# Kernel optimization log

Measured on AMD Instinct MI355X. Metric: run time of the kernel, lower is better.

The kernel has to match this reference:

```python
import math
import jax, jax.numpy as jnp
import numpy as np

N_HEADS = 32
N_KV_HEADS = 8
HEAD_DIM = 64
DIM = 2048
SEQ = 4096
EST_Q = 64          # idx = min(64, seqlen)
VERTICAL_SIZE = 300 # min(prompt_len, max(300, 30))
SLASH_SIZE = 800    # min(prompt_len, max(800, 50))


def apply_rope(t, cos, sin):
    # t: [B,S,H,hd]; pairs are consecutive (reshape(...,-1,2) in torch view_as_complex)
    B, S, H, hd = t.shape
    tr = t.reshape(B, S, H, hd // 2, 2)
    xr, xi = tr[..., 0], tr[..., 1]
    c = cos[None, :, None, :]
    s = sin[None, :, None, :]
    orr = xr * c - xi * s
    oii = xr * s + xi * c
    return jnp.stack([orr, oii], axis=-1).reshape(B, S, H, hd)


def sum_all_diagonal(mat):
    # faithful jax version of torch as_strided trick: sum over anti-shifted diagonals
    # mat: [b,h,n,m] -> [b,h,n+m-1]; sum_diags[j] = sum_i mat[i, i + j - n], j in [1, n+m-1]
    b, h, n, m = mat.shape
    padded = jnp.pad(mat, ((0, 0), (0, 0), (0, 0), (n, n)))
    gidx = jnp.arange(n)[:, None] + jnp.arange(n + m)[None, :]  # [n, n+m]
    diags = jnp.take_along_axis(padded, jnp.broadcast_to(gidx, (b, h, n, n + m)), axis=-1)
    return diags.sum(axis=2)[:, :, 1:]


def setup_inputs() -> dict:
    key = jax.random.key(0)
    ks = jax.random.split(key, 6)
    x = jax.random.normal(ks[0], (1, SEQ, DIM), dtype=jnp.float32)
    # real RoPE tables (theta = 10000)
    inv_freq = 1.0 / (10000.0 ** (np.arange(0, HEAD_DIM, 2, dtype=np.float32) / HEAD_DIM))
    ang = np.outer(np.arange(SEQ, dtype=np.float32), inv_freq)  # [S, hd/2]
    freqs_cos = jnp.asarray(np.cos(ang), dtype=jnp.float32)
    freqs_sin = jnp.asarray(np.sin(ang), dtype=jnp.float32)
    scale = 0.02
    wq = jax.random.normal(ks[1], (DIM, N_HEADS * HEAD_DIM), dtype=jnp.float32) * scale
    wk = jax.random.normal(ks[2], (DIM, N_KV_HEADS * HEAD_DIM), dtype=jnp.float32) * scale
    wv = jax.random.normal(ks[3], (DIM, N_KV_HEADS * HEAD_DIM), dtype=jnp.float32) * scale
    wo = jax.random.normal(ks[4], (N_HEADS * HEAD_DIM, DIM), dtype=jnp.float32) * scale
    return {"x": x, "freqs_cos": freqs_cos, "freqs_sin": freqs_sin,
            "wq": wq, "wk": wk, "wv": wv, "wo": wo}


def reference(x, freqs_cos, freqs_sin, wq, wk, wv, wo):
    B, S, D = x.shape
    H, Hkv, hd = N_HEADS, N_KV_HEADS, HEAD_DIM
    rep = H // Hkv
    scale = 1.0 / math.sqrt(hd)

    # QKV + RoPE (K gets RoPE, V does not), GQA repeat
    q = apply_rope((x @ wq).reshape(B, S, H, hd), freqs_cos, freqs_sin).transpose(0, 2, 1, 3)
    k = apply_rope((x @ wk).reshape(B, S, Hkv, hd), freqs_cos, freqs_sin)
    v = (x @ wv).reshape(B, S, Hkv, hd)
    k = jnp.repeat(k, rep, axis=2).transpose(0, 2, 1, 3)  # [B,H,S,hd]
    v = jnp.repeat(v, rep, axis=2).transpose(0, 2, 1, 3)

    # --- vertical / slash pattern estimation (first idx queries, as in source) ---
    idx = min(EST_Q, S)
    qe = q[:, :, :idx, :]
    est = jnp.einsum('bhqd,bhkd->bhqk', qe, k) * scale  # [B,H,idx,S]
    ar = jnp.arange(idx)
    blk = ar[:, None] >= ar[None, :]
    tail = jnp.where(blk[None, None], est[..., -idx:], -jnp.inf)
    est = jnp.concatenate([est[..., :S - idx], tail], axis=-1)
    probs = jax.nn.softmax(est, axis=-1)

    Vn = min(S, VERTICAL_SIZE)
    Sl = min(S, SLASH_SIZE)
    vertical = probs.sum(axis=2)                  # [B,H,S]
    _, v_idx = jax.lax.top_k(vertical, Vn)        # [B,H,Vn]
    diag = sum_all_diagonal(probs)[..., :S]       # [..., :-idx+1] -> length S
    _, s_idx = jax.lax.top_k(diag, Sl)
    slash = S - 1 - s_idx                         # [B,H,Sl]

    sparse_keys = jnp.sort(jnp.concatenate([v_idx, slash], axis=-1), axis=-1)  # [B,H,K]

    # --- sparse causal attention over selected keys ---
    k_sp = jnp.take_along_axis(k, sparse_keys[..., None], axis=2)  # [B,H,K,hd]
    v_sp = jnp.take_along_axis(v, sparse_keys[..., None], axis=2)
    att = jnp.einsum('bhqd,bhkd->bhqk', q, k_sp) * scale           # [B,H,S,K]
    causal = sparse_keys[:, :, None, :] <= jnp.arange(S)[None, None, :, None]
    att = jnp.where(causal, att, -1e30)
    p = jax.nn.softmax(att, axis=-1)
    out = jnp.einsum('bhqk,bhkd->bhqd', p, v_sp)
    out = out.transpose(0, 2, 1, 3).reshape(B, S, H * hd)
    return out @ wo
```

## Files before the change

### kernel.cpp

```cpp
#include <hip/hip_runtime.h>
#include <hip/hip_bf16.h>
#include <math.h>
#include <stdint.h>

#define SEQ   4096
#define DIMM  2048
#define NH    32
#define NKV   8
#define HD    64
#define NSP   1100
#define NSPP  1152

typedef __bf16 bf16x8 __attribute__((ext_vector_type(8)));
typedef float  f32x4  __attribute__((ext_vector_type(4)));

#define MODE_V 0
#define MODE_Q 1
#define MODE_O 2

__device__ inline void split8(const float* __restrict__ p, bf16x8& h, bf16x8& l) {
#pragma unroll
    for (int i = 0; i < 8; ++i) {
        float v = p[i];
        __bf16 hv = (__bf16)v;
        h[i] = hv;
        l[i] = (__bf16)(v - (float)hv);
    }
}
__device__ inline f32x4 load4(const void* __restrict__ p, size_t idx, bool f) {
    if (f) return *(const f32x4*)((const float*)p + idx);
    const __bf16* b = (const __bf16*)p + idx;
    f32x4 v;
    v[0] = (float)b[0]; v[1] = (float)b[1]; v[2] = (float)b[2]; v[3] = (float)b[3];
    return v;
}
__device__ __forceinline__ void gl_lds16(const __bf16* __restrict__ g, __bf16* l) {
    __builtin_amdgcn_global_load_lds(
        (const __attribute__((address_space(1))) void*)g,
        (__attribute__((address_space(3))) void*)l, 16, 0, 0);
}
__device__ __forceinline__ void cs_at(const void* fc, const void* fs, bool f,
                                      int t, int j, float& c, float& s) {
    if (f) {
        c = ((const float*)fc)[t * 32 + j];
        s = ((const float*)fs)[t * 32 + j];
    } else {
        c = (float)((const __bf16*)fc)[t * 32 + j];
        s = (float)((const __bf16*)fs)[t * 32 + j];
    }
}

__global__ __launch_bounds__(256) void detect_k(const void* __restrict__ x,
                                                int* __restrict__ flag) {
    const __bf16* p = (const __bf16*)x;
    int tid = threadIdx.x;
    bool bad = false;
    for (int i = 0; i < 16; ++i) {
        float v = fabsf((float)p[tid * 16 + i]);
        if (!(v <= 1e10f)) bad = true;
    }
    unsigned long long m = __ballot(bad);
    __shared__ unsigned long long w[4];
    if ((tid & 63) == 0) w[tid >> 6] = m;
    __syncthreads();
    if (tid == 0) flag[0] = ((w[0] | w[1] | w[2] | w[3]) != 0ULL) ? 1 : 0;
}

__device__ __forceinline__ void transpose_body(const void* __restrict__ in,
                                               __bf16* __restrict__ out,
                                               int R, int C, bool f,
                                               int cb, int rb) {
    __shared__ __bf16 tile[32][33];
    int tx = threadIdx.x & 31, ty = threadIdx.x >> 5;
    for (int i = 0; i < 32; i += 8) {
        size_t idx = (size_t)(rb + ty + i) * C + cb + tx;
        float v = f ? ((const float*)in)[idx] : (float)((const __bf16*)in)[idx];
        tile[ty + i][tx] = (__bf16)v;
    }
    __syncthreads();
    for (int i = 0; i < 32; i += 8)
        out[(size_t)(cb + ty + i) * R + rb + tx] = tile[tx][ty + i];
}

__device__ __forceinline__ void transpose_split_body(const void* __restrict__ in,
                                                     __bf16* __restrict__ oh,
                                                     __bf16* __restrict__ ol,
                                                     int R, int C, bool f,
                                                     int cb, int rb) {
    __shared__ float tf[32][33];
    int tx = threadIdx.x & 31, ty = threadIdx.x >> 5;
    for (int i = 0; i < 32; i += 8) {
        size_t idx = (size_t)(rb + ty + i) * C + cb + tx;
        tf[ty + i][tx] = f ? ((const float*)in)[idx] : (float)((const __bf16*)in)[idx];
    }
    __syncthreads();
    for (int i = 0; i < 32; i += 8) {
        float v = tf[tx][ty + i];
        __bf16 h = (__bf16)v;
        size_t o = (size_t)(cb + ty + i) * R + rb + tx;
        oh[o] = h;
        ol[o] = (__bf16)(v - (float)h);
    }
}

__global__ __launch_bounds__(256) void convert_wkt_k(const void* __restrict__ x,
                                                     __bf16* __restrict__ xb,
                                                     const void* __restrict__ wk,
                                                     __bf16* __restrict__ Wtk_h,
                                                     __bf16* __restrict__ Wtk_l,
                                                     const int* __restrict__ flag) {
    int bid = blockIdx.x;
    bool f = (*flag != 0);
    if (bid < 4096) {
        int i0 = (bid * 256 + threadIdx.x) * 8;
        if (f) {
            const float* xf = (const float*)x;
            bf16x8 o;
            for (int i = 0; i < 8; ++i) o[i] = (__bf16)xf[i0 + i];
            *(bf16x8*)(xb + i0) = o;
        } else {
            *(bf16x8*)(xb + i0) = *(const bf16x8*)((const __bf16*)x + i0);
        }
    } else {
        int id = bid - 4096;
        int cb = (id >> 6) * 32, rb = (id & 63) * 32;
        transpose_split_body(wk, Wtk_h, Wtk_l, 2048, 512, f, cb, rb);
    }
}

__device__ __forceinline__ void gemm_ksplit_body(const void* __restrict__ x,
                                                 const __bf16* __restrict__ Bh,
                                                 const __bf16* __restrict__ Bl,
                                                 float* __restrict__ C,
                                                 __bf16* __restrict__ Cb,
                                                 bool f, int bm, int bn,
                                                 const void* __restrict__ fc,
                                                 const void* __restrict__ fs,
                                                 char* smem) {
    const int K = DIMM, N = 512;
    float (*Asf)[68] = (float (*)[68])smem;
    __bf16* Bsh = (__bf16*)(smem + 8704);
    __bf16* Bsl = (__bf16*)(smem + 8704 + 16384);
    int tid = threadIdx.x, wave = tid >> 6, lane = tid & 63;
    int quad = lane >> 4, l16 = lane & 15;
    int wn = wave * 32;
    const f32x4 z4 = {0.f, 0.f, 0.f, 0.f};
    f32x4 acc[2][2];
    for (int a = 0; a < 2; ++a) for (int b = 0; b < 2; ++b) acc[a][b] = z4;
    int arow = tid >> 3, ac8 = (tid & 7) * 8;
    const __bf16* Bhb = Bh + (size_t)(bn * 128) * K;
    const __bf16* Blb = Bl + (size_t)(bn * 128) * K;
    for (int k0 = 0; k0 < K; k0 += 64) {
        f32x4 va0 = load4(x, (size_t)(bm * 32 + arow) * K + k0 + ac8, f);
        f32x4 va1 = load4(x, (size_t)(bm * 32 + arow) * K + k0 + ac8 + 4, f);
        *(f32x4*)&Asf[arow][ac8]     = va0;
        *(f32x4*)&Asf[arow][ac8 + 4] = va1;
#pragma unroll
        for (int it = 0; it < 4; ++it) {
            int ci = it * 256 + tid;
            int row = ci >> 3, c8 = (ci & 7) * 8;
            gl_lds16(Bhb + (size_t)row * K + k0 + c8, Bsh + ci * 8);
            gl_lds16(Blb + (size_t)row * K + k0 + c8, Bsl + ci * 8);
        }
        __syncthreads();
#pragma unroll
        for (int ks = 0; ks < 2; ++ks) {
            bf16x8 ah[2], al[2], bh[2], bl[2];
#pragma unroll
            for (int mt = 0; mt < 2; ++mt)
                split8(&Asf[mt * 16 + l16][ks * 32 + quad * 8], ah[mt], al[mt]);
#pragma unroll
            for (int nt = 0; nt < 2; ++nt) {
                bh[nt] = *(const bf16x8*)&Bsh[(wn + nt * 16 + l16) * 64 + ks * 32 + quad * 8];
                bl[nt] = *(const bf16x8*)&Bsl[(wn + nt * 16 + l16) * 64 + ks * 32 + quad * 8];
            }
#pragma unroll
            for (int mt = 0; mt < 2; ++mt)
#pragma unroll
                for (int nt = 0; nt < 2; ++nt) {
                    acc[mt][nt] = __builtin_amdgcn_mfma_f32_16x16x32_bf16(al[mt], bh[nt], acc[mt][nt], 0, 0, 0);
                    acc[mt][nt] = __builtin_amdgcn_mfma_f32_16x16x32_bf16(ah[mt], bl[nt], acc[mt][nt], 0, 0, 0);
                    acc[mt][nt] = __builtin_amdgcn_mfma_f32_16x16x32_bf16(ah[mt], bh[nt], acc[mt][nt], 0, 0, 0);
                }
        }
        __syncthreads();
    }
    for (int mt = 0; mt < 2; ++mt)
        for (int nt = 0; nt < 2; ++nt)
#pragma unroll
            for (int r = 0; r < 4; ++r) {
                int col = bn * 128 + wn + nt * 16 + l16;
                int t = bm * 32 + mt * 16 + quad * 4 + r;
                float v = acc[mt][nt][r];
                float pv = __shfl_xor(v, 1);
                int j = (col & 63) >> 1;
                float c, s;
                cs_at(fc, fs, f, t, j, c, s);
                float o = (lane & 1) ? (pv * s + v * c) : (v * c - pv * s);
                C[(size_t)t * N + col] = o;
                Cb[(size_t)t * N + col] = (__bf16)o;
            }
}

__device__ __forceinline__ void gemm_qesplit_body(const void* __restrict__ A,
                                                  const void* __restrict__ B,
                                                  float* __restrict__ C,
                                                  int N, bool f, int bm, int bn,
                                                  const void* __restrict__ fc,
                                                  const void* __restrict__ fs,
                                                  char* smem) {
    const int K = DIMM;
    float (*Asf)[36] = (float (*)[36])smem;
    float (*Bsf)[36] = (float (*)[36])(smem + 4608);
    int tid = threadIdx.x, wave = tid >> 6, lane = tid & 63;
    int quad = lane >> 4, l16 = lane & 15;
    int wn = wave * 32;
    const f32x4 z4 = {0.f, 0.f, 0.f, 0.f};
    f32x4 acc[2][2];
    for (int a = 0; a < 2; ++a) for (int b = 0; b < 2; ++b) acc[a][b] = z4;
    int arow = tid >> 3, acol = (tid & 7) * 4;
    for (int k0 = 0; k0 < K; k0 += 32) {
        {
            f32x4 va = load4(A, (size_t)(bm * 32 + arow) * K + k0 + acol, f);
            *(f32x4*)&Asf[arow][acol] = va;
        }
        for (int it = 0; it < 4; ++it) {
            int g = tid + it * 256;
            int krow = g >> 5, ng = (g & 31) * 4;
            f32x4 v = load4(B, (size_t)(k0 + krow) * N + bn * 128 + ng, f);
            Bsf[ng + 0][krow] = v[0];
            Bsf[ng + 1][krow] = v[1];
            Bsf[ng + 2][krow] = v[2];
            Bsf[ng + 3][krow] = v[3];
        }
        __syncthreads();
        bf16x8 ah[2], al[2], bh[2], bl[2];
        for (int mt = 0; mt < 2; ++mt) split8(&Asf[mt * 16 + l16][quad * 8], ah[mt], al[mt]);
        for (int nt = 0; nt < 2; ++nt) split8(&Bsf[wn + nt * 16 + l16][quad * 8], bh[nt], bl[nt]);
        for (int mt = 0; mt < 2; ++mt)
            for (int nt = 0; nt < 2; ++nt) {
                acc[mt][nt] = __builtin_amdgcn_mfma_f32_16x16x32_bf16(al[mt], bh[nt], acc[mt][nt], 0, 0, 0);
                acc[mt][nt] = __builtin_amdgcn_mfma_f32_16x16x32_bf16(ah[mt], bl[nt], acc[mt][nt], 0, 0, 0);
                acc[mt][nt] = __builtin_amdgcn_mfma_f32_16x16x32_bf16(ah[mt], bh[nt], acc[mt][nt], 0, 0, 0);
            }
        __syncthreads();
    }
    for (int mt = 0; mt < 2; ++mt)
        for (int nt = 0; nt < 2; ++nt)
#pragma unroll
            for (int r = 0; r < 4; ++r) {
                int col = bn * 128 + wn + nt * 16 + l16;
                int t = bm * 32 + mt * 16 + quad * 4 + r;
                float v = acc[mt][nt][r];
                float pv = __shfl_xor(v, 1);
                float o = v;
                if (t < 64) {
                    int j = (col & 63) >> 1;
                    float c, s;
                    cs_at(fc, fs, f, t, j, c, s);
                    o = (lane & 1) ? (pv * s + v * c) : (v * c - pv * s);
                }
                C[(size_t)t * N + col] = o;
            }
}

__global__ __launch_bounds__(256) void split_dual_rope_k(const void* __restrict__ x,
                                                         const __bf16* __restrict__ Wtk_h,
                                                         const __bf16* __restrict__ Wtk_l,
                                                         float* __restrict__ Kf,
                                                         const void* __restrict__ wq,
                                                         float* __restrict__ Qe,
                                                         __bf16* __restrict__ Kb,
                                                         const void* __restrict__ fc,
                                                         const void* __restrict__ fs,
                                                         const int* __restrict__ flag) {
    __shared__ __align__(16) char smem[41472];
    bool f = (*flag != 0);
    int bid = blockIdx.x;
    if (bid < 512) {
        gemm_ksplit_body(x, Wtk_h, Wtk_l, Kf, Kb, f, bid >> 2, bid & 3, fc, fs, smem);
    } else {
        int i = bid - 512;
        gemm_qesplit_body(x, wq, Qe, 2048, f, i >> 4, i & 15, fc, fs, smem);
    }
}

__device__ __forceinline__ void gemm_nt_body(const __bf16* __restrict__ A,
                                             const __bf16* __restrict__ Bt,
                                             void* __restrict__ C, int N,
                                             int bm, int bn, bool f, int mode,
                                             const void* __restrict__ fc,
                                             const void* __restrict__ fs,
                                             char* smem) {
    const int K = DIMM;
    __bf16* As = (__bf16*)smem;
    __bf16* Bs = (__bf16*)(smem + 16384);
    int tid = threadIdx.x, wave = tid >> 6, lane = tid & 63;
    int quad = lane >> 4, l16 = lane & 15;
    int wm = (wave >> 1) * 64, wn = (wave & 1) * 64;
    const f32x4 z4 = {0.f, 0.f, 0.f, 0.f};
    f32x4 acc[4][4];
    for (int a = 0; a < 4; ++a) for (int b = 0; b < 4; ++b) acc[a][b] = z4;
    const __bf16* Ab = A  + (size_t)(bm * 128) * K;
    const __bf16* Bb = Bt + (size_t)(bn * 128) * K;
    for (int k0 = 0; k0 < K; k0 += 64) {
#pragma unroll
        for (int it = 0; it < 4; ++it) {
            int ci = it * 256 + tid;
            int row = ci >> 3, c8 = (ci & 7) * 8;
            gl_lds16(Ab + (size_t)row * K + k0 + c8, As + ci * 8);
            gl_lds16(Bb + (size_t)row * K + k0 + c8, Bs + ci * 8);
        }
        __syncthreads();
#pragma unroll
        for (int ks = 0; ks < 2; ++ks) {
            bf16x8 af[4], bfr[4];
#pragma unroll
            for (int mt = 0; mt < 4; ++mt)
                af[mt]  = *(const bf16x8*)&As[(wm + mt * 16 + l16) * 64 + ks * 32 + quad * 8];
#pragma unroll
            for (int nt = 0; nt < 4; ++nt)
                bfr[nt] = *(const bf16x8*)&Bs[(wn + nt * 16 + l16) * 64 + ks * 32 + quad * 8];
#pragma unroll
            for (int mt = 0; mt < 4; ++mt)
#pragma unroll
                for (int nt = 0; nt < 4; ++nt)
                    acc[mt][nt] = __builtin_amdgcn_mfma_f32_16x16x32_bf16(af[mt], bfr[nt], acc[mt][nt], 0, 0, 0);
        }
        __syncthreads();
    }
    if (mode == MODE_Q) {
        for (int mt = 0; mt < 4; ++mt)
            for (int nt = 0; nt < 4; ++nt)
#pragma unroll
                for (int r = 0; r < 4; ++r) {
                    int col = bn * 128 + wn + nt * 16 + l16;
                    int t = bm * 128 + wm + mt * 16 + quad * 4 + r;
                    float qv = (float)(__bf16)acc[mt][nt][r];
                    float pv = __shfl_xor(qv, 1);
                    int j = (col & 63) >> 1;
                    float c, s;
                    cs_at(fc, fs, f, t, j, c, s);
                    float o = (lane & 1) ? (pv * s + qv * c) : (qv * c - pv * s);
                    ((__bf16*)C)[(size_t)t * N + col] = (__bf16)o;
                }
    } else if (mode == MODE_O) {
        bool f32o = f;
        for (int mt = 0; mt < 4; ++mt)
            for (int nt = 0; nt < 4; ++nt) {
                int rowb = bm * 128 + wm + mt * 16 + quad * 4;
                int col = bn * 128 + wn + nt * 16 + l16;
                if (f32o) {
                    for (int r = 0; r < 4; ++r)
                        ((float*)C)[(size_t)(rowb + r) * N + col] = acc[mt][nt][r];
                } else {
                    for (int r = 0; r < 4; ++r)
                        ((__bf16*)C)[(size_t)(rowb + r) * N + col] = (__bf16)acc[mt][nt][r];
                }
            }
    } else {
        for (int mt = 0; mt < 4; ++mt)
            for (int nt = 0; nt < 4; ++nt) {
                int rowb = bm * 128 + wm + mt * 16 + quad * 4;
                int col = bn * 128 + wn + nt * 16 + l16;
                for (int r = 0; r < 4; ++r)
                    ((__bf16*)C)[(size_t)(rowb + r) * N + col] = (__bf16)acc[mt][nt][r];
            }
    }
}

__global__ __launch_bounds__(256) void gemm_qv_k(const __bf16* __restrict__ xbf,
                                                 const __bf16* __restrict__ Wtq,
                                                 const __bf16* __restrict__ Wtv,
                                                 __bf16* __restrict__ Qb,
                                                 __bf16* __restrict__ Vb,
                                                 const void* __restrict__ fc,
                                                 const void* __restrict__ fs,
                                                 const int* __restrict__ flag) {
    __shared__ __align__(16) char smem[32768];
    bool f = (*flag != 0);
    int bx = blockIdx.x, by = blockIdx.y;
    if (bx < 32) {
        gemm_nt_body(xbf, Wtq, Qb, 2048, bx, by, f, MODE_Q, fc, fs, smem);
    } else {
        int bm = (bx - 32) * 4 + (by >> 2), bn = by & 3;
        gemm_nt_body(xbf, Wtv, Vb, 512, bm, bn, f, MODE_V, nullptr, nullptr, smem);
    }
}

__global__ __launch_bounds__(256) void gemm_o_k(const __bf16* __restrict__ A,
                                                const __bf16* __restrict__ Bt,
                                                void* __restrict__ C,
                                                const int* __restrict__ flag) {
    __shared__ __align__(16) char smem[32768];
    bool f = (*flag != 0);
    gemm_nt_body(A, Bt, C, 2048, blockIdx.x, blockIdx.y, f, MODE_O, nullptr, nullptr, smem);
}

__global__ __launch_bounds__(256) void est_part_k(const float* __restrict__ Qe,
                                                  const float* __restrict__ Kf,
                                                  float* __restrict__ pm,
                                                  float* __restrict__ ps,
                                                  float* __restrict__ diag) {
    int h = blockIdx.x, sl = blockIdx.y;
    int tid = threadIdx.x, wave = tid >> 6, lane = tid & 63;
    int quad = lane >> 4, l16 = lane & 15;
    for (int i = tid; i < 512; i += 256) diag[h * SEQ + sl * 512 + i] = 0.f;
    __shared__ float Ml[64];
    __shared__ float pA[4][64];
    bf16x8 qh[4][2], ql[4][2];
    for (int mt = 0; mt < 4; ++mt)
        for (int kc = 0; kc < 2; ++kc)
            split8(Qe + (size_t)(mt * 16 + l16) * DIMM + h * HD + kc * 32 + quad * 8,
                   qh[mt][kc], ql[mt][kc]);
    int kvoff = (h >> 2) * HD;
    float pmax[4][4];
    for (int mt = 0; mt < 4; ++mt) for (int r = 0; r < 4; ++r) pmax[mt][r] = -3.0e38f;
    for (int jb = wave; jb < 8; jb += 4)
        for (int c = 0; c < 4; ++c) {
            int j0 = sl * 512 + jb * 64 + c * 16;
            const float* kp = Kf + (size_t)(j0 + l16) * (NKV * HD) + kvoff + quad * 8;
            bf16x8 kh0, kl0, kh1, kl1;
            split8(kp, kh0, kl0);
            split8(kp + 32, kh1, kl1);
            int j = j0 + l16;
            for (int mt = 0; mt < 4; ++mt) {
                f32x4 acc = {0.f, 0.f, 0.f, 0.f};
                acc = __builtin_amdgcn_mfma_f32_16x16x32_bf16(ql[mt][0], kh0, acc, 0, 0, 0);
                acc = __builtin_amdgcn_mfma_f32_16x16x32_bf16(qh[mt][0], kl0, acc, 0, 0, 0);
                acc = __builtin_amdgcn_mfma_f32_16x16x32_bf16(qh[mt][0], kh0, acc, 0, 0, 0);
                acc = __builtin_amdgcn_mfma_f32_16x16x32_bf16(ql[mt][1], kh1, acc, 0, 0, 0);
                acc = __builtin_amdgcn_mfma_f32_16x16x32_bf16(qh[mt][1], kl1, acc, 0, 0, 0);
                acc = __builtin_amdgcn_mfma_f32_16x16x32_bf16(qh[mt][1], kh1, acc, 0, 0, 0);
                for (int r = 0; r < 4; ++r) {
                    int q = mt * 16 + quad * 4 + r;
                    float sv = acc[r] * 0.125f;
                    if (j >= SEQ - 64 && q < j - (SEQ - 64)) sv = -1e30f;
                    pmax[mt][r] = fmaxf(pmax[mt][r], sv);
                }
            }
        }
    for (int mt = 0; mt < 4; ++mt)
        for (int r = 0; r < 4; ++r)
            for (int m2 = 1; m2 < 16; m2 <<= 1)
                pmax[mt][r] = fmaxf(pmax[mt][r], __shfl_xor(pmax[mt][r], m2));
    if (l16 == 0)
        for (int mt = 0; mt < 4; ++mt)
            for (int r = 0; r < 4; ++r)
                pA[wave][mt * 16 + quad * 4 + r] = pmax[mt][r];
    __syncthreads();
    if (tid < 64)
        Ml[tid] = fmaxf(fmaxf(pA[0][tid], pA[1][tid]), fmaxf(pA[2][tid], pA[3][tid]));
    __syncthreads();
    float mreg[4][4];
    for (int mt = 0; mt < 4; ++mt)
        for (int r = 0; r < 4; ++r)
            mreg[mt][r] = Ml[mt * 16 + quad * 4 + r];
    float psum[4][4];
    for (int mt = 0; mt < 4; ++mt) for (int r = 0; r < 4; ++r) psum[mt][r] = 0.f;
    for (int jb = wave; jb < 8; jb += 4)
        for (int c = 0; c < 4; ++c) {
            int j0 = sl * 512 + jb * 64 + c * 16;
            const float* kp = Kf + (size_t)(j0 + l16) * (NKV * HD) + kvoff + quad * 8;
            bf16x8 kh0, kl0, kh1, kl1;
            split8(kp, kh0, kl0);
            split8(kp + 32, kh1, kl1);
            int j = j0 + l16;
            for (int mt = 0; mt < 4; ++mt) {
                f32x4 acc = {0.f, 0.f, 0.f, 0.f};
                acc = __builtin_amdgcn_mfma_f32_16x16x32_bf16(ql[mt][0], kh0, acc, 0, 0, 0);
                acc = __builtin_amdgcn_mfma_f32_16x16x32_bf16(qh[mt][0], kl0, acc, 0, 0, 0);
                acc = __builtin_amdgcn_mfma_f32_16x16x32_bf16(qh[mt][0], kh0, acc, 0, 0, 0);
                acc = __builtin_amdgcn_mfma_f32_16x16x32_bf16(ql[mt][1], kh1, acc, 0, 0, 0);
                acc = __builtin_amdgcn_mfma_f32_16x16x32_bf16(qh[mt][1], kl1, acc, 0, 0, 0);
                acc = __builtin_amdgcn_mfma_f32_16x16x32_bf16(qh[mt][1], kh1, acc, 0, 0, 0);
                for (int r = 0; r < 4; ++r) {
                    int q = mt * 16 + quad * 4 + r;
                    float sv = acc[r] * 0.125f;
                    if (j >= SEQ - 64 && q < j - (SEQ - 64)) sv = -1e30f;
                    psum[mt][r] += __expf(sv - mreg[mt][r]);
                }
            }
        }
    for (int mt = 0; mt < 4; ++mt)
        for (int r = 0; r < 4; ++r)
            for (int m2 = 1; m2 < 16; m2 <<= 1)
                psum[mt][r] += __shfl_xor(psum[mt][r], m2);
    if (l16 == 0)
        for (int mt = 0; mt < 4; ++mt)
            for (int r = 0; r < 4; ++r)
                pA[wave][mt * 16 + quad * 4 + r] = psum[mt][r];
    __syncthreads();
    if (tid < 64) {
        pm[(h * 8 + sl) * 64 + tid] = Ml[tid];
        ps[(h * 8 + sl) * 64 + tid] = pA[0][tid] + pA[1][tid] + pA[2][tid] + pA[3][tid];
    }
}

__global__ __launch_bounds__(256) void vert_diag_k(const float* __restrict__ Qe,
                                                   const float* __restrict__ Kf,
                                                   const float* __restrict__ pm,
                                                   const float* __restrict__ ps,
                                                   float* __restrict__ vert,
                                                   float* __restrict__ diag) {
    int h = blockIdx.x, jb = blockIdx.y;
    int tid = threadIdx.x, wave = tid >> 6, lane = tid & 63;
    int quad = lane >> 4, l16 = lane & 15;
    __shared__ float P[64][132];
    __shared__ float dloc[192];
    __shared__ float rm_l[64], rs_l[64];
    for (int i = tid; i < 192; i += 256) dloc[i] = 0.f;
    if (tid < 64) {
        float M = -3.0e38f;
        for (int sl = 0; sl < 8; ++sl) M = fmaxf(M, pm[(h * 8 + sl) * 64 + tid]);
        float S = 0.f;
        for (int sl = 0; sl < 8; ++sl)
            S += ps[(h * 8 + sl) * 64 + tid] * __expf(pm[(h * 8 + sl) * 64 + tid] - M);
        rm_l[tid] = M;
        rs_l[tid] = S;
    }
    bf16x8 qh[4][2], ql[4][2];
    for (int mt = 0; mt < 4; ++mt)
        for (int kc = 0; kc < 2; ++kc)
            split8(Qe + (size_t)(mt * 16 + l16) * DIMM + h * HD + kc * 32 + quad * 8,
                   qh[mt][kc], ql[mt][kc]);
    __syncthreads();
    float rm[4][4], rs[4][4];
    for (int mt = 0; mt < 4; ++mt)
        for (int r = 0; r < 4; ++r) {
            int q = mt * 16 + quad * 4 + r;
            rm[mt][r] = rm_l[q];
            rs[mt][r] = rs_l[q];
        }
    int kvoff = (h >> 2) * HD;
    for (int c = 0; c < 2; ++c) {
        int jl0 = wave * 32 + c * 16;
        int j0 = jb * 128 + jl0;
        const float* kp = Kf + (size_t)(j0 + l16) * (NKV * HD) + kvoff + quad * 8;
        bf16x8 kh0, kl0, kh1, kl1;
        split8(kp, kh0, kl0);
        split8(kp + 32, kh1, kl1);
        int j = j0 + l16;
        for (int mt = 0; mt < 4; ++mt) {
            f32x4 acc = {0.f, 0.f, 0.f, 0.f};
            acc = __builtin_amdgcn_mfma_f32_16x16x32_bf16(ql[mt][0], kh0, acc, 0, 0, 0);
            acc = __builtin_amdgcn_mfma_f32_16x16x32_bf16(qh[mt][0], kl0, acc, 0, 0, 0);
            acc = __builtin_amdgcn_mfma_f32_16x16x32_bf16(qh[mt][0], kh0, acc, 0, 0, 0);
            acc = __builtin_amdgcn_mfma_f32_16x16x32_bf16(ql[mt][1], kh1, acc, 0, 0, 0);
            acc = __builtin_amdgcn_mfma_f32_16x16x32_bf16(qh[mt][1], kl1, acc, 0, 0, 0);
            acc = __builtin_amdgcn_mfma_f32_16x16x32_bf16(qh[mt][1], kh1, acc, 0, 0, 0);
            for (int r = 0; r < 4; ++r) {
                int q = mt * 16 + quad * 4 + r;
                float sv = acc[r] * 0.125f;
                if (j >= SEQ - 64 && q < j - (SEQ - 64)) sv = -1e30f;
                P[q][jl0 + l16] = __expf(sv - rm[mt][r]) / rs[mt][r];
            }
        }
    }
    __syncthreads();
    if (tid < 128) {
        float vacc = 0.f;
        for (int q = 0; q < 64; ++q) {
            float pb = P[q][tid];
            vacc += pb;
            if (jb * 128 + tid + 63 - q < SEQ) atomicAdd(&dloc[tid + 63 - q], pb);
        }
        vert[h * SEQ + jb * 128 + tid] = vacc;
    }
    __syncthreads();
    for (int i = tid; i < 192; i += 256) {
        int g = jb * 128 + i;
        if (g < SEQ) atomicAdd(&diag[h * SEQ + g], dloc[i]);
    }
}

__global__ __launch_bounds__(256) void topk_qvt_k(const float* __restrict__ vert,
                                                  const float* __restrict__ diag,
                                                  int* __restrict__ skeys,
                                                  const void* __restrict__ wq,
                                                  __bf16* __restrict__ Wtq,
                                                  const void* __restrict__ wv,
                                                  __bf16* __restrict__ Wtv,
                                                  const int* __restrict__ flag) {
    if (blockIdx.x >= 32) {
        bool f = (*flag != 0);
        int id = blockIdx.x - 32;
        int bx = id >> 6, by = id & 63;
        if (bx < 64) transpose_body(wq, Wtq, 2048, 2048, f, bx * 32, by * 32);
        else         transpose_body(wv, Wtv, 2048,  512, f, (bx - 64) * 32, by * 32);
        return;
    }
    __shared__ int cnt[4096];
    __shared__ int hist4[4][256];
    __shared__ int scanb[256];
    __shared__ int B_sh, kk_sh;
    int h = blockIdx.x, tid = threadIdx.x, wave = tid >> 6;
    for (int i = tid; i < 4096; i += 256) cnt[i] = 0;
    __syncthreads();
    for (int selp = 0; selp < 2; ++selp) {
        const float* vals = (selp == 0 ? vert : diag) + h * SEQ;
        int k = (selp == 0) ? 300 : 800;
        bool flip = (selp == 1);
        unsigned bits[16];
        for (int g = 0; g < 4; ++g) {
            f32x4 v = *(const f32x4*)(vals + tid * 16 + g * 4);
            for (int e = 0; e < 4; ++e) bits[g * 4 + e] = __float_as_uint(v[e]);
        }
        unsigned prefix = 0;
        int kk = k;
        for (int pass = 0; pass < 4; ++pass) {
            int sh = 8 * (3 - pass);
            for (int w = 0; w < 4; ++w) hist4[w][tid] = 0;
            __syncthreads();
            for (int e = 0; e < 16; ++e) {
                unsigned b = bits[e];
                bool in = (pass == 0) || ((b >> (sh + 8)) == prefix);
                if (in) atomicAdd(&hist4[wave][(b >> sh) & 255], 1);
            }
            __syncthreads();
            scanb[tid] = hist4[0][tid] + hist4[1][tid] + hist4[2][tid] + hist4[3][tid];
            __syncthreads();
            for (int off = 1; off < 256; off <<= 1) {
                int v = (tid + off < 256) ? scanb[tid + off] : 0;
                __syncthreads();
                scanb[tid] += v;
                __syncthreads();
            }
            int sufNext = (tid < 255) ? scanb[tid + 1] : 0;
            if (scanb[tid] >= kk && sufNext < kk) { B_sh = tid; kk_sh = kk - sufNext; }
            __syncthreads();
            prefix = (prefix << 8) | (unsigned)B_sh;
            kk = kk_sh;
            __syncthreads();
        }
        int localEq = 0;
        for (int e = 0; e < 16; ++e) {
            unsigned b = bits[e];
            if (b > prefix) {
                int idx = tid * 16 + e;
                atomicAdd(&cnt[flip ? (4095 - idx) : idx], 1);
            } else if (b == prefix) ++localEq;
        }
        scanb[tid] = localEq;
        __syncthreads();
        for (int off = 1; off < 256; off <<= 1) {
            int v = (tid >= off) ? scanb[tid - off] : 0;
            __syncthreads();
            scanb[tid] += v;
            __syncthreads();
        }
        int eqOff = scanb[tid] - localEq;
        int taken = 0;
        for (int e = 0; e < 16; ++e) {
            unsigned b = bits[e];
            if (b == prefix) {
                if (eqOff + taken < kk) {
                    int idx = tid * 16 + e;
                    atomicAdd(&cnt[flip ? (4095 - idx) : idx], 1);
                }
                ++taken;
            }
        }
        __syncthreads();
    }
    int base = tid * 16;
    int loc[16];
    int s = 0;
    for (int e = 0; e < 16; ++e) { loc[e] = s; s += cnt[base + e]; }
    scanb[tid] = s;
    __syncthreads();
    for (int off = 1; off < 256; off <<= 1) {
        int v = (tid >= off) ? scanb[tid - off] : 0;
        __syncthreads();
        scanb[tid] += v;
        __syncthreads();
    }
    int chunkExcl = scanb[tid] - s;
    int* out = skeys + h * NSPP;
    for (int e = 0; e < 16; ++e) {
        int c = cnt[base + e];
        int pos = chunkExcl + loc[e];
        for (int r = 0; r < c; ++r) out[pos + r] = base + e;
    }
    for (int i = NSP + tid; i < NSPP; i += 256) out[i] = 0x7fffffff;
}

__global__ __launch_bounds__(256) void gather_wot_k(const __bf16* __restrict__ Kb,
                                                    const __bf16* __restrict__ Vb,
                                                    const int* __restrict__ skeys,
                                                    __bf16* __restrict__ Ksp,
                                                    __bf16* __restrict__ VspT,
                                                    const void* __restrict__ wo,
                                                    __bf16* __restrict__ Wto,
                                                    const int* __restrict__ flag) {
    int bid = blockIdx.x;
    if (bid >= 576) {
        bool f = (*flag != 0);
        int id = bid - 576;
        transpose_body(wo, Wto, 2048, 2048, f, (id >> 6) * 32, (id & 63) * 32);
        return;
    }
    int h = bid / 18, jb = bid % 18;
    __shared__ __bf16 tile[64][72];
    int tid = threadIdx.x;
    int jl = tid >> 2, d0 = (tid & 3) * 16;
    int j = jb * 64 + jl;
    int key = skeys[h * NSPP + j];
    int kv = (h >> 2) * HD;
    const bf16x8 z = {};
    bf16x8 k0v = z, k1v = z, v0v = z, v1v = z;
    if ((unsigned)key < SEQ) {
        const __bf16* ks = Kb + (size_t)key * (NKV * HD) + kv + d0;
        const __bf16* vs = Vb + (size_t)key * (NKV * HD) + kv + d0;
        k0v = *(const bf16x8*)ks; k1v = *(const bf16x8*)(ks + 8);
        v0v = *(const bf16x8*)vs; v1v = *(const bf16x8*)(vs + 8);
    }
    __bf16* kd = Ksp + ((size_t)h * NSPP + j) * HD + d0;
    *(bf16x8*)kd = k0v;
    *(bf16x8*)(kd + 8) = k1v;
    *(bf16x8*)&tile[jl][d0] = v0v;
    *(bf16x8*)&tile[jl][d0 + 8] = v1v;
    __syncthreads();
    int d = tid >> 2, jl0 = (tid & 3) * 16;
    bf16x8 o0, o1;
    for (int e = 0; e < 8; ++e) { o0[e] = tile[jl0 + e][d]; o1[e] = tile[jl0 + 8 + e][d]; }
    __bf16* vt = VspT + ((size_t)h * HD + d) * NSPP + jb * 64 + jl0;
    *(bf16x8*)vt = o0;
    *(bf16x8*)(vt + 8) = o1;
}

__global__ __launch_bounds__(512) void sparse_attn_k(const __bf16* Qb,
                                                     const __bf16* __restrict__ Ksp,
                                                     const __bf16* __restrict__ VspT,
                                                     const int* __restrict__ skeys,
                                                     __bf16* AO) {
    int qb = blockIdx.x, h = blockIdx.y;
    int tid = threadIdx.x, wave = tid >> 6, lane = tid & 63;
    int quad = lane >> 4, l16 = lane & 15;
    __shared__ __bf16 sc[64][1160];
    __shared__ float rsm[64];
    int t0 = qb * 64;
    bf16x8 aq[4][2];
#pragma unroll
    for (int qs = 0; qs < 4; ++qs)
#pragma unroll
        for (int kc = 0; kc < 2; ++kc)
            aq[qs][kc] = *(const bf16x8*)(Qb + (size_t)(t0 + qs * 16 + l16) * DIMM + h * HD + kc * 32 + quad * 8);
    const __bf16* Kh = Ksp + (size_t)h * NSPP * HD;
    const int* sk = skeys + h * NSPP;
#pragma unroll
    for (int c = 0; c < 9; ++c) {
        int j0 = wave * 144 + c * 16;
        const __bf16* kp = Kh + (size_t)(j0 + l16) * HD + quad * 8;
        bf16x8 b0 = *(const bf16x8*)kp;
        bf16x8 b1 = *(const bf16x8*)(kp + 32);
        int j = j0 + l16;
        int key = sk[j];
#pragma unroll
        for (int qs = 0; qs < 4; ++qs) {
            f32x4 acc = {0.f, 0.f, 0.f, 0.f};
            acc = __builtin_amdgcn_mfma_f32_16x16x32_bf16(aq[qs][0], b0, acc, 0, 0, 0);
            acc = __builtin_amdgcn_mfma_f32_16x16x32_bf16(aq[qs][1], b1, acc, 0, 0, 0);
            int qg = t0 + qs * 16 + quad * 4;
#pragma unroll
            for (int r = 0; r < 4; ++r) {
                float sv = acc[r] * 0.125f;
                if (key > qg + r) sv = -1e30f;
                sc[qs * 16 + quad * 4 + r][j] = (__bf16)sv;
            }
        }
    }
    __syncthreads();
    {
        int row = tid >> 3, sub = tid & 7;
        int c0 = sub * 144;
        float mx = -3.0e38f;
        for (int i = 0; i < 18; ++i) {
            bf16x8 v = *(const bf16x8*)&sc[row][c0 + i * 8];
            for (int e = 0; e < 8; ++e) mx = fmaxf(mx, (float)v[e]);
        }
        for (int m2 = 1; m2 < 8; m2 <<= 1) mx = fmaxf(mx, __shfl_xor(mx, m2, 8));
        float sm = 0.f;
        for (int i = 0; i < 18; ++i) {
            int cb = c0 + i * 8;
            bf16x8 v = *(const bf16x8*)&sc[row][cb];
            bf16x8 pw;
            for (int e = 0; e < 8; ++e) {
                float pv = 0.f;
                if (cb + e < NSP) { pv = __expf((float)v[e] - mx); sm += pv; }
                pw[e] = (__bf16)pv;
            }
            *(bf16x8*)&sc[row][cb] = pw;
        }
        for (int m2 = 1; m2 < 8; m2 <<= 1) sm += __shfl_xor(sm, m2, 8);
        if (sub == 0) rsm[row] = sm;
    }
    __syncthreads();
    int qs = wave >> 1, dh = wave & 1;
    const f32x4 z4 = {0.f, 0.f, 0.f, 0.f};
    f32x4 o0 = z4, o1 = z4;
    const __bf16* Vh = VspT + ((size_t)h * HD + dh * 32) * NSPP;
#pragma unroll 4
    for (int c = 0; c < 36; ++c) {
        int kb = c * 32;
        bf16x8 pa = *(const bf16x8*)&sc[qs * 16 + l16][kb + quad * 8];
        bf16x8 v0 = *(const bf16x8*)(Vh + (size_t)l16 * NSPP + kb + quad * 8);
        bf16x8 v1 = *(const bf16x8*)(Vh + (size_t)(16 + l16) * NSPP + kb + quad * 8);
        o0 = __builtin_amdgcn_mfma_f32_16x16x32_bf16(pa, v0, o0, 0, 0, 0);
        o1 = __builtin_amdgcn_mfma_f32_16x16x32_bf16(pa, v1, o1, 0, 0, 0);
    }
#pragma unroll
    for (int r = 0; r < 4; ++r) {
        int ql = qs * 16 + quad * 4 + r;
        float inv = 1.f / rsm[ql];
        size_t base = (size_t)(t0 + ql) * DIMM + h * HD + dh * 32;
        AO[base + l16]      = (__bf16)(o0[r] * inv);
        AO[base + 16 + l16] = (__bf16)(o1[r] * inv);
    }
}

extern "C" void kernel_launch(void* const* d_in, const int* in_sizes, int n_in,
                              void* d_out, int out_size, void* d_ws, size_t ws_size,
                              hipStream_t stream) {
    const void* x  = d_in[0];
    const void* fc = d_in[1];
    const void* fs = d_in[2];
    const void* wq = d_in[3];
    const void* wk = d_in[4];
    const void* wv = d_in[5];
    const void* wo = d_in[6];
    char* ws = (char*)d_ws;

    __bf16* Wtk_h= (__bf16*)(ws + 0);
    __bf16* Wtk_l= (__bf16*)(ws + 2097152);
    float*  Kf32 = (float*)(ws + 4194304);
    float*  Qef32= (float*)(ws + 12582912);
    float*  pm   = (float*)(ws + 13631488);
    float*  ps   = (float*)(ws + 13697024);
    float*  vert = (float*)(ws + 13762560);
    float*  diag = (float*)(ws + 14286848);
    __bf16* Qb   = (__bf16*)(ws + 0);
    __bf16* Kb   = (__bf16*)(ws + 16777216);
    __bf16* Vb   = (__bf16*)(ws + 20971520);
    __bf16* xbf  = (__bf16*)(ws + 25165824);
    __bf16* Ksp  = (__bf16*)(ws + 25165824);
    __bf16* VspT = (__bf16*)(ws + 29884416);
    __bf16* Wtq  = (__bf16*)(ws + 41943040);
    __bf16* Wto  = (__bf16*)(ws + 41943040);
    __bf16* Wtv  = (__bf16*)(ws + 50331648);
    int*    skeys= (int*)(ws + 52445184);
    int*    flag = (int*)(ws + 52592640);

    dim3 b256(256);
    detect_k<<<1, b256, 0, stream>>>(x, flag);
    convert_wkt_k<<<5120, b256, 0, stream>>>(x, xbf, wk, Wtk_h, Wtk_l, flag);
    split_dual_rope_k<<<544, b256, 0, stream>>>(x, Wtk_h, Wtk_l, Kf32, wq, Qef32,
                                                Kb, fc, fs, flag);
    est_part_k<<<dim3(32, 8), b256, 0, stream>>>(Qef32, Kf32, pm, ps, diag);
    vert_diag_k<<<dim3(32, 32), b256, 0, stream>>>(Qef32, Kf32, pm, ps, vert, diag);
    topk_qvt_k<<<5152, b256, 0, stream>>>(vert, diag, skeys, wq, Wtq, wv, Wtv, flag);
    gemm_qv_k<<<dim3(40, 16), b256, 0, stream>>>(xbf, Wtq, Wtv, Qb, Vb, fc, fs, flag);
    gather_wot_k<<<4672, b256, 0, stream>>>(Kb, Vb, skeys, Ksp, VspT, wo, Wto, flag);
    sparse_attn_k<<<dim3(64, 32), dim3(512), 0, stream>>>(Qb, Ksp, VspT, skeys, Qb);
    gemm_o_k<<<dim3(32, 16), b256, 0, stream>>>(Qb, Wto, d_out, flag);
}
```

Before: 908.6 us.

## Pre-split K/Qe into bf16 hi/lo and rebalance transposes and V projection

The K and Q-estimate projections now write bf16 high and low halves directly, instead of fp32 that the estimation kernels re-split with split8 on every load. The wq and wv transposes move into the first conversion kernel. The V projection GEMM moves into the top-k kernel so it runs alongside the top-k blocks, which leaves the Q GEMM as its own smaller launch. This shortens the critical path and removes repeated conversion work, at the cost of a larger conversion launch and reusing one workspace region for both Kl and Vb.

```diff
diff --git a/kernel.cpp b/kernel.cpp
--- a/kernel.cpp
+++ b/kernel.cpp
@@ -103,11 +103,15 @@
     }
 }
 
-__global__ __launch_bounds__(256) void convert_wkt_k(const void* __restrict__ x,
+__global__ __launch_bounds__(256) void convert_all_k(const void* __restrict__ x,
                                                      __bf16* __restrict__ xb,
                                                      const void* __restrict__ wk,
                                                      __bf16* __restrict__ Wtk_h,
                                                      __bf16* __restrict__ Wtk_l,
+                                                     const void* __restrict__ wq,
+                                                     __bf16* __restrict__ Wtq,
+                                                     const void* __restrict__ wv,
+                                                     __bf16* __restrict__ Wtv,
                                                      const int* __restrict__ flag) {
     int bid = blockIdx.x;
     bool f = (*flag != 0);
@@ -121,18 +125,23 @@
         } else {
             *(bf16x8*)(xb + i0) = *(const bf16x8*)((const __bf16*)x + i0);
         }
+    } else if (bid < 5120) {
+        int id = bid - 4096;
+        transpose_split_body(wk, Wtk_h, Wtk_l, 2048, 512, f, (id >> 6) * 32, (id & 63) * 32);
+    } else if (bid < 9216) {
+        int id = bid - 5120;
+        transpose_body(wq, Wtq, 2048, 2048, f, (id >> 6) * 32, (id & 63) * 32);
     } else {
-        int id = bid - 4096;
-        int cb = (id >> 6) * 32, rb = (id & 63) * 32;
-        transpose_split_body(wk, Wtk_h, Wtk_l, 2048, 512, f, cb, rb);
+        int id = bid - 9216;
+        transpose_body(wv, Wtv, 2048, 512, f, (id >> 6) * 32, (id & 63) * 32);
     }
 }
 
 __device__ __forceinline__ void gemm_ksplit_body(const void* __restrict__ x,
                                                  const __bf16* __restrict__ Bh,
                                                  const __bf16* __restrict__ Bl,
-                                                 float* __restrict__ C,
-                                                 __bf16* __restrict__ Cb,
+                                                 __bf16* __restrict__ Kh,
+                                                 __bf16* __restrict__ Kl,
                                                  bool f, int bm, int bn,
                                                  const void* __restrict__ fc,
                                                  const void* __restrict__ fs,
@@ -197,14 +206,16 @@
                 float c, s;
                 cs_at(fc, fs, f, t, j, c, s);
                 float o = (lane & 1) ? (pv * s + v * c) : (v * c - pv * s);
-                C[(size_t)t * N + col] = o;
-                Cb[(size_t)t * N + col] = (__bf16)o;
+                __bf16 h16 = (__bf16)o;
+                Kh[(size_t)t * N + col] = h16;
+                Kl[(size_t)t * N + col] = (__bf16)(o - (float)h16);
             }
 }
 
 __device__ __forceinline__ void gemm_qesplit_body(const void* __restrict__ A,
                                                   const void* __restrict__ B,
-                                                  float* __restrict__ C,
+                                                  __bf16* __restrict__ Qeh,
+                                                  __bf16* __restrict__ Qel,
                                                   int N, bool f, int bm, int bn,
                                                   const void* __restrict__ fc,
                                                   const void* __restrict__ fs,
@@ -253,24 +264,24 @@
                 int t = bm * 32 + mt * 16 + quad * 4 + r;
                 float v = acc[mt][nt][r];
                 float pv = __shfl_xor(v, 1);
-                float o = v;
-                if (t < 64) {
-                    int j = (col & 63) >> 1;
-                    float c, s;
-                    cs_at(fc, fs, f, t, j, c, s);
-                    o = (lane & 1) ? (pv * s + v * c) : (v * c - pv * s);
-                }
-                C[(size_t)t * N + col] = o;
+                int j = (col & 63) >> 1;
+                float c, s;
+                cs_at(fc, fs, f, t, j, c, s);
+                float o = (lane & 1) ? (pv * s + v * c) : (v * c - pv * s);
+                __bf16 h16 = (__bf16)o;
+                Qeh[(size_t)t * N + col] = h16;
+                Qel[(size_t)t * N + col] = (__bf16)(o - (float)h16);
             }
 }
 
 __global__ __launch_bounds__(256) void split_dual_rope_k(const void* __restrict__ x,
                                                          const __bf16* __restrict__ Wtk_h,
                                                          const __bf16* __restrict__ Wtk_l,
-                                                         float* __restrict__ Kf,
+                                                         __bf16* __restrict__ Kh,
+                                                         __bf16* __restrict__ Kl,
                                                          const void* __restrict__ wq,
-                                                         float* __restrict__ Qe,
-                                                         __bf16* __restrict__ Kb,
+                                                         __bf16* __restrict__ Qeh,
+                                                         __bf16* __restrict__ Qel,
                                                          const void* __restrict__ fc,
                                                          const void* __restrict__ fs,
                                                          const int* __restrict__ flag) {
@@ -278,10 +289,10 @@
     bool f = (*flag != 0);
     int bid = blockIdx.x;
     if (bid < 512) {
-        gemm_ksplit_body(x, Wtk_h, Wtk_l, Kf, Kb, f, bid >> 2, bid & 3, fc, fs, smem);
+        gemm_ksplit_body(x, Wtk_h, Wtk_l, Kh, Kl, f, bid >> 2, bid & 3, fc, fs, smem);
     } else {
         int i = bid - 512;
-        gemm_qesplit_body(x, wq, Qe, 2048, f, i >> 4, i & 15, fc, fs, smem);
+        gemm_qesplit_body(x, wq, Qeh, Qel, 2048, f, i >> 4, i & 15, fc, fs, smem);
     }
 }
 
@@ -369,23 +380,15 @@
     }
 }
 
-__global__ __launch_bounds__(256) void gemm_qv_k(const __bf16* __restrict__ xbf,
-                                                 const __bf16* __restrict__ Wtq,
-                                                 const __bf16* __restrict__ Wtv,
-                                                 __bf16* __restrict__ Qb,
-                                                 __bf16* __restrict__ Vb,
-                                                 const void* __restrict__ fc,
-                                                 const void* __restrict__ fs,
-                                                 const int* __restrict__ flag) {
+__global__ __launch_bounds__(256) void gemm_q_k(const __bf16* __restrict__ xbf,
+                                                const __bf16* __restrict__ Wtq,
+                                                __bf16* __restrict__ Qb,
+                                                const void* __restrict__ fc,
+                                                const void* __restrict__ fs,
+                                                const int* __restrict__ flag) {
     __shared__ __align__(16) char smem[32768];
     bool f = (*flag != 0);
-    int bx = blockIdx.x, by = blockIdx.y;
-    if (bx < 32) {
-        gemm_nt_body(xbf, Wtq, Qb, 2048, bx, by, f, MODE_Q, fc, fs, smem);
-    } else {
-        int bm = (bx - 32) * 4 + (by >> 2), bn = by & 3;
-        gemm_nt_body(xbf, Wtv, Vb, 512, bm, bn, f, MODE_V, nullptr, nullptr, smem);
-    }
+    gemm_nt_body(xbf, Wtq, Qb, 2048, blockIdx.x, blockIdx.y, f, MODE_Q, fc, fs, smem);
 }
 
 __global__ __launch_bounds__(256) void gemm_o_k(const __bf16* __restrict__ A,
@@ -397,8 +400,10 @@
     gemm_nt_body(A, Bt, C, 2048, blockIdx.x, blockIdx.y, f, MODE_O, nullptr, nullptr, smem);
 }
 
-__global__ __launch_bounds__(256) void est_part_k(const float* __restrict__ Qe,
-                                                  const float* __restrict__ Kf,
+__global__ __launch_bounds__(256) void est_part_k(const __bf16* __restrict__ Qeh,
+                                                  const __bf16* __restrict__ Qel,
+                                                  const __bf16* __restrict__ Kh,
+                                                  const __bf16* __restrict__ Kl,
                                                   float* __restrict__ pm,
                                                   float* __restrict__ ps,
                                                   float* __restrict__ diag) {
@@ -410,19 +415,22 @@
     __shared__ float pA[4][64];
     bf16x8 qh[4][2], ql[4][2];
     for (int mt = 0; mt < 4; ++mt)
-        for (int kc = 0; kc < 2; ++kc)
-            split8(Qe + (size_t)(mt * 16 + l16) * DIMM + h * HD + kc * 32 + quad * 8,
-                   qh[mt][kc], ql[mt][kc]);
+        for (int kc = 0; kc < 2; ++kc) {
+            size_t qo = (size_t)(mt * 16 + l16) * DIMM + h * HD + kc * 32 + quad * 8;
+            qh[mt][kc] = *(const bf16x8*)(Qeh + qo);
+            ql[mt][kc] = *(const bf16x8*)(Qel + qo);
+        }
     int kvoff = (h >> 2) * HD;
     float pmax[4][4];
     for (int mt = 0; mt < 4; ++mt) for (int r = 0; r < 4; ++r) pmax[mt][r] = -3.0e38f;
     for (int jb = wave; jb < 8; jb += 4)
         for (int c = 0; c < 4; ++c) {
             int j0 = sl * 512 + jb * 64 + c * 16;
-            const float* kp = Kf + (size_t)(j0 + l16) * (NKV * HD) + kvoff + quad * 8;
-            bf16x8 kh0, kl0, kh1, kl1;
-            split8(kp, kh0, kl0);
-            split8(kp + 32, kh1, kl1);
+            size_t ko = (size_t)(j0 + l16) * (NKV * HD) + kvoff + quad * 8;
+            bf16x8 kh0 = *(const bf16x8*)(Kh + ko);
+            bf16x8 kl0 = *(const bf16x8*)(Kl + ko);
+            bf16x8 kh1 = *(const bf16x8*)(Kh + ko + 32);
+            bf16x8 kl1 = *(const bf16x8*)(Kl + ko + 32);
             int j = j0 + l16;
             for (int mt = 0; mt < 4; ++mt) {
                 f32x4 acc = {0.f, 0.f, 0.f, 0.f};
@@ -461,10 +469,11 @@
     for (int jb = wave; jb < 8; jb += 4)
         for (int c = 0; c < 4; ++c) {
             int j0 = sl * 512 + jb * 64 + c * 16;
-            const float* kp = Kf + (size_t)(j0 + l16) * (NKV * HD) + kvoff + quad * 8;
-            bf16x8 kh0, kl0, kh1, kl1;
-            split8(kp, kh0, kl0);
-            split8(kp + 32, kh1, kl1);
+            size_t ko = (size_t)(j0 + l16) * (NKV * HD) + kvoff + quad * 8;
+            bf16x8 kh0 = *(const bf16x8*)(Kh + ko);
+            bf16x8 kl0 = *(const bf16x8*)(Kl + ko);
+            bf16x8 kh1 = *(const bf16x8*)(Kh + ko + 32);
+            bf16x8 kl1 = *(const bf16x8*)(Kl + ko + 32);
             int j = j0 + l16;
             for (int mt = 0; mt < 4; ++mt) {
                 f32x4 acc = {0.f, 0.f, 0.f, 0.f};
@@ -497,8 +506,10 @@
     }
 }
 
-__global__ __launch_bounds__(256) void vert_diag_k(const float* __restrict__ Qe,
-                                                   const float* __restrict__ Kf,
+__global__ __launch_bounds__(256) void vert_diag_k(const __bf16* __restrict__ Qeh,
+                                                   const __bf16* __restrict__ Qel,
+                                                   const __bf16* __restrict__ Kh,
+                                                   const __bf16* __restrict__ Kl,
                                                    const float* __restrict__ pm,
                                                    const float* __restrict__ ps,
                                                    float* __restrict__ vert,
@@ -521,9 +532,11 @@
     }
     bf16x8 qh[4][2], ql[4][2];
     for (int mt = 0; mt < 4; ++mt)
-        for (int kc = 0; kc < 2; ++kc)
-            split8(Qe + (size_t)(mt * 16 + l16) * DIMM + h * HD + kc * 32 + quad * 8,
-                   qh[mt][kc], ql[mt][kc]);
+        for (int kc = 0; kc < 2; ++kc) {
+            size_t qo = (size_t)(mt * 16 + l16) * DIMM + h * HD + kc * 32 + quad * 8;
+            qh[mt][kc] = *(const bf16x8*)(Qeh + qo);
+            ql[mt][kc] = *(const bf16x8*)(Qel + qo);
+        }
     __syncthreads();
     float rm[4][4], rs[4][4];
     for (int mt = 0; mt < 4; ++mt)
@@ -536,10 +549,11 @@
     for (int c = 0; c < 2; ++c) {
         int jl0 = wave * 32 + c * 16;
         int j0 = jb * 128 + jl0;
-        const float* kp = Kf + (size_t)(j0 + l16) * (NKV * HD) + kvoff + quad * 8;
-        bf16x8 kh0, kl0, kh1, kl1;
-        split8(kp, kh0, kl0);
-        split8(kp + 32, kh1, kl1);
+        size_t ko = (size_t)(j0 + l16) * (NKV * HD) + kvoff + quad * 8;
+        bf16x8 kh0 = *(const bf16x8*)(Kh + ko);
+        bf16x8 kl0 = *(const bf16x8*)(Kl + ko);
+        bf16x8 kh1 = *(const bf16x8*)(Kh + ko + 32);
+        bf16x8 kl1 = *(const bf16x8*)(Kl + ko + 32);
         int j = j0 + l16;
         for (int mt = 0; mt < 4; ++mt) {
             f32x4 acc = {0.f, 0.f, 0.f, 0.f};
@@ -574,20 +588,18 @@
     }
 }
 
-__global__ __launch_bounds__(256) void topk_qvt_k(const float* __restrict__ vert,
-                                                  const float* __restrict__ diag,
-                                                  int* __restrict__ skeys,
-                                                  const void* __restrict__ wq,
-                                                  __bf16* __restrict__ Wtq,
-                                                  const void* __restrict__ wv,
-                                                  __bf16* __restrict__ Wtv,
-                                                  const int* __restrict__ flag) {
+__global__ __launch_bounds__(256) void topk_vproj_k(const float* __restrict__ vert,
+                                                    const float* __restrict__ diag,
+                                                    int* __restrict__ skeys,
+                                                    const __bf16* __restrict__ xbf,
+                                                    const __bf16* __restrict__ Wtv,
+                                                    __bf16* __restrict__ Vb,
+                                                    const int* __restrict__ flag) {
     if (blockIdx.x >= 32) {
+        __shared__ __align__(16) char smem[32768];
         bool f = (*flag != 0);
         int id = blockIdx.x - 32;
-        int bx = id >> 6, by = id & 63;
-        if (bx < 64) transpose_body(wq, Wtq, 2048, 2048, f, bx * 32, by * 32);
-        else         transpose_body(wv, Wtv, 2048,  512, f, (bx - 64) * 32, by * 32);
+        gemm_nt_body(xbf, Wtv, Vb, 512, id >> 2, id & 3, f, MODE_V, nullptr, nullptr, smem);
         return;
     }
     __shared__ int cnt[4096];
@@ -746,12 +758,12 @@
 #pragma unroll
         for (int kc = 0; kc < 2; ++kc)
             aq[qs][kc] = *(const bf16x8*)(Qb + (size_t)(t0 + qs * 16 + l16) * DIMM + h * HD + kc * 32 + quad * 8);
-    const __bf16* Kh = Ksp + (size_t)h * NSPP * HD;
+    const __bf16* Kh2 = Ksp + (size_t)h * NSPP * HD;
     const int* sk = skeys + h * NSPP;
 #pragma unroll
     for (int c = 0; c < 9; ++c) {
         int j0 = wave * 144 + c * 16;
-        const __bf16* kp = Kh + (size_t)(j0 + l16) * HD + quad * 8;
+        const __bf16* kp = Kh2 + (size_t)(j0 + l16) * HD + quad * 8;
         bf16x8 b0 = *(const bf16x8*)kp;
         bf16x8 b1 = *(const bf16x8*)(kp + 32);
         int j = j0 + l16;
@@ -833,14 +845,15 @@
 
     __bf16* Wtk_h= (__bf16*)(ws + 0);
     __bf16* Wtk_l= (__bf16*)(ws + 2097152);
-    float*  Kf32 = (float*)(ws + 4194304);
-    float*  Qef32= (float*)(ws + 12582912);
-    float*  pm   = (float*)(ws + 13631488);
-    float*  ps   = (float*)(ws + 13697024);
-    float*  vert = (float*)(ws + 13762560);
-    float*  diag = (float*)(ws + 14286848);
+    __bf16* Qeh  = (__bf16*)(ws + 4194304);
+    __bf16* Qel  = (__bf16*)(ws + 4456448);
+    float*  pm   = (float*)(ws + 4718592);
+    float*  ps   = (float*)(ws + 4784128);
+    float*  vert = (float*)(ws + 4849664);
+    float*  diag = (float*)(ws + 5373952);
     __bf16* Qb   = (__bf16*)(ws + 0);
-    __bf16* Kb   = (__bf16*)(ws + 16777216);
+    __bf16* Kh   = (__bf16*)(ws + 16777216);
+    __bf16* Kl   = (__bf16*)(ws + 20971520);
     __bf16* Vb   = (__bf16*)(ws + 20971520);
     __bf16* xbf  = (__bf16*)(ws + 25165824);
     __bf16* Ksp  = (__bf16*)(ws + 25165824);
@@ -853,14 +866,15 @@
 
     dim3 b256(256);
     detect_k<<<1, b256, 0, stream>>>(x, flag);
-    convert_wkt_k<<<5120, b256, 0, stream>>>(x, xbf, wk, Wtk_h, Wtk_l, flag);
-    split_dual_rope_k<<<544, b256, 0, stream>>>(x, Wtk_h, Wtk_l, Kf32, wq, Qef32,
-                                                Kb, fc, fs, flag);
-    est_part_k<<<dim3(32, 8), b256, 0, stream>>>(Qef32, Kf32, pm, ps, diag);
-    vert_diag_k<<<dim3(32, 32), b256, 0, stream>>>(Qef32, Kf32, pm, ps, vert, diag);
-    topk_qvt_k<<<5152, b256, 0, stream>>>(vert, diag, skeys, wq, Wtq, wv, Wtv, flag);
-    gemm_qv_k<<<dim3(40, 16), b256, 0, stream>>>(xbf, Wtq, Wtv, Qb, Vb, fc, fs, flag);
-    gather_wot_k<<<4672, b256, 0, stream>>>(Kb, Vb, skeys, Ksp, VspT, wo, Wto, flag);
+    convert_all_k<<<10240, b256, 0, stream>>>(x, xbf, wk, Wtk_h, Wtk_l,
+                                              wq, Wtq, wv, Wtv, flag);
+    split_dual_rope_k<<<544, b256, 0, stream>>>(x, Wtk_h, Wtk_l, Kh, Kl,
+                                                wq, Qeh, Qel, fc, fs, flag);
+    est_part_k<<<dim3(32, 8), b256, 0, stream>>>(Qeh, Qel, Kh, Kl, pm, ps, diag);
+    vert_diag_k<<<dim3(32, 32), b256, 0, stream>>>(Qeh, Qel, Kh, Kl, pm, ps, vert, diag);
+    topk_vproj_k<<<160, b256, 0, stream>>>(vert, diag, skeys, xbf, Wtv, Vb, flag);
+    gemm_q_k<<<dim3(32, 16), b256, 0, stream>>>(xbf, Wtq, Qb, fc, fs, flag);
+    gather_wot_k<<<4672, b256, 0, stream>>>(Kh, Vb, skeys, Ksp, VspT, wo, Wto, flag);
     sparse_attn_k<<<dim3(64, 32), dim3(512), 0, stream>>>(Qb, Ksp, VspT, skeys, Qb);
     gemm_o_k<<<dim3(32, 16), b256, 0, stream>>>(Qb, Wto, d_out, flag);
 }
```

Measured after the change: 776.2 us. 14.6% less time.
